# Kernel optimization log

Measured on AMD Instinct MI355X. Metric: run time of the kernel, lower is better.

Reference implementation:

```python
import jax, jax.numpy as jnp
import numpy as np

GRADIENT_SCALE = 1.0  # undefined global in the source; standard surrogate scale
ALPHA = 0.9
BETA = 0.8
THRESHOLD = 1.0
FEATURES = 512
UNITS = 1024
TIME = 256
BATCH = 128

@jax.custom_vjp
def heaviside(x):
    return jnp.where(x > 0, jnp.ones_like(x), jnp.zeros_like(x))

def _heaviside_fwd(x):
    return heaviside(x), x

def _heaviside_bwd(x, dy):
    # dy * GRADIENT_SCALE * (1/(|x|+1))^2  (surrogate gradient from tf.custom_gradient)
    return (dy * (GRADIENT_SCALE * jnp.square(1.0 / (jnp.abs(x) + 1.0))),)

heaviside.defvjp(_heaviside_fwd, _heaviside_bwd)


def setup_inputs() -> dict:
    key = jax.random.key(0)
    k1, k2 = jax.random.split(key)
    inputs = jax.random.normal(k1, (BATCH, FEATURES, TIME), dtype=jnp.float32)
    # keras add_weight default initializer ~ glorot_uniform; any float init is fine for a numerics baseline
    limit = np.sqrt(6.0 / (FEATURES + UNITS)).astype(np.float32)
    w = jax.random.uniform(k2, (FEATURES, UNITS), dtype=jnp.float32, minval=-limit, maxval=limit)
    return {"inputs": inputs, "w": w}


def reference(inputs, w):
    # In the original tf.while_loop body, membrane_potential, synapse and prev_s are
    # returned UNMODIFIED, so they remain zero for every timestep. The recurrence
    # therefore collapses exactly to, per step t:
    #   h_t = x[:, :, t] @ w
    #   i_t = alpha*0 + h_t = h_t
    #   v_t = (beta*0 + h_t) * (threshold - 0) = h_t * threshold
    #   s_t = heaviside(v_t - threshold)
    # which is timestep-independent and can be computed as one batched GEMM.
    h = jnp.einsum('bft,fu->btu', inputs, w)        # [B, T, U]
    v = (BETA * 0.0 + h) * (THRESHOLD - 0.0)        # state terms are identically zero
    s = heaviside(v - THRESHOLD)                    # [B, T, U]
    return jnp.transpose(s, (0, 2, 1))              # [B, U, T], matching tf transpose perm=[1,2,0]
```

## Files before the change

### kernel.cpp

```cpp
#include <hip/hip_runtime.h>


#define FF 512
#define TT 256
#define UU 1024
#define BK 8
#define MW 32

typedef float floatx16 __attribute__((ext_vector_type(16)));

__global__ __launch_bounds__(256, 6)
void snn_gemm_r5(const float* __restrict__ in, const float* __restrict__ w,
                 float* __restrict__ out) {
    const int b   = blockIdx.y;
    const int u0  = blockIdx.x * MW;
    const int tid = threadIdx.x;

    const float* __restrict__ inb = in + (size_t)b * FF * TT + tid;

    float acc[MW];
#pragma unroll
    for (int i = 0; i < MW; i++) acc[i] = 0.0f;

    float cur[BK], nxt[BK];
#pragma unroll
    for (int r = 0; r < BK; r++) cur[r] = inb[(size_t)r * TT];

    for (int f0 = 0; f0 < FF; f0 += BK) {
        if (f0 + BK < FF) {
#pragma unroll
            for (int r = 0; r < BK; r++)
                nxt[r] = inb[(size_t)(f0 + BK + r) * TT];
        }

#pragma unroll
        for (int k = 0; k < BK; k++) {
            const floatx16* __restrict__ pa =
                (const floatx16*)(w + (size_t)(f0 + k) * UU + u0);
            const floatx16 aL = pa[0];
            const floatx16 aH = pa[1];

            const float vb = cur[k];

#pragma unroll
            for (int i = 0; i < 16; i++)
                acc[i] = fmaf(aL[i], vb, acc[i]);
#pragma unroll
            for (int i = 0; i < 16; i++)
                acc[16 + i] = fmaf(aH[i], vb, acc[16 + i]);
        }

#pragma unroll
        for (int r = 0; r < BK; r++) cur[r] = nxt[r];
    }

    float* __restrict__ outb = out + ((size_t)b * UU + u0) * TT + tid;
#pragma unroll
    for (int i = 0; i < MW; i++)
        outb[(size_t)i * TT] = acc[i] > 1.0f ? 1.0f : 0.0f;
}

extern "C" void kernel_launch(void* const* d_in, const int* in_sizes, int n_in,
                              void* d_out, int out_size, void* d_ws, size_t ws_size,
                              hipStream_t stream) {
    const float* in = (const float*)d_in[0];
    const float* w  = (const float*)d_in[1];
    float* out      = (float*)d_out;

    dim3 grid(UU / MW, 128);
    snn_gemm_r5<<<grid, dim3(256), 0, stream>>>(in, w, out);
}
```

Baseline: 587.0 us.

## Restructure GEMM into LDS-tiled 128x64 blocks with async global-to-LDS double buffering

Replaces the per-thread column GEMM, where each thread kept 32 accumulators and streamed the weights through scalar or vector loads, with a 128(U) x 64(T) block tile. Each thread now computes a 16x8 register micro-tile from operands staged in shared memory, so each loaded value is reused across many FMAs. Tiles are loaded with global_load_lds into double-buffered LDS, and the output is written as float4 stores. The cost is higher register pressure (launch bounds drop to 2 blocks per CU) and a block-wide barrier every k-step, with no explicit wait on the async loads before the barrier.

```diff
diff --git a/kernel.cpp b/kernel.cpp
--- a/kernel.cpp
+++ b/kernel.cpp
@@ -5,59 +5,93 @@
 #define TT 256
 #define UU 1024
 #define BK 8
-#define MW 32
 
-typedef float floatx16 __attribute__((ext_vector_type(16)));
+__global__ __launch_bounds__(256, 2)
+void snn_gemm_r6(const float* __restrict__ in, const float* __restrict__ w,
+                 float* __restrict__ out) {
+    __shared__ float As[2][BK][128];
+    __shared__ float Bs[2][BK][64];
 
-__global__ __launch_bounds__(256, 6)
-void snn_gemm_r5(const float* __restrict__ in, const float* __restrict__ w,
-                 float* __restrict__ out) {
-    const int b   = blockIdx.y;
-    const int u0  = blockIdx.x * MW;
-    const int tid = threadIdx.x;
+    const int b    = blockIdx.z;
+    const int u0   = blockIdx.y * 128;
+    const int t0   = blockIdx.x * 64;
+    const int tid  = threadIdx.x;
+    const int wv   = tid >> 6;
+    const int lane = tid & 63;
+    const int g    = lane >> 3;
+    const int h    = lane & 7;
 
-    const float* __restrict__ inb = in + (size_t)b * FF * TT + tid;
+    const float* __restrict__ inb = in + (size_t)b * FF * TT;
 
-    float acc[MW];
+    float acc[16][8];
 #pragma unroll
-    for (int i = 0; i < MW; i++) acc[i] = 0.0f;
+    for (int i = 0; i < 16; i++)
+#pragma unroll
+        for (int j = 0; j < 8; j++) acc[i][j] = 0.0f;
 
-    float cur[BK], nxt[BK];
-#pragma unroll
-    for (int r = 0; r < BK; r++) cur[r] = inb[(size_t)r * TT];
+#define STAGE(fn, buf)                                                          \
+    do {                                                                        \
+        __builtin_amdgcn_global_load_lds(                                       \
+            (const __attribute__((address_space(1))) void*)                     \
+                (w + (size_t)((fn) + 2 * wv + (lane >> 5)) * UU + u0 +          \
+                 (lane & 31) * 4),                                              \
+            (__attribute__((address_space(3))) void*)&As[buf][2 * wv][0],       \
+            16, 0, 0);                                                          \
+        if (wv < 2) {                                                           \
+            __builtin_amdgcn_global_load_lds(                                   \
+                (const __attribute__((address_space(1))) void*)                 \
+                    (inb + (size_t)((fn) + 4 * wv + (lane >> 4)) * TT + t0 +    \
+                     (lane & 15) * 4),                                          \
+                (__attribute__((address_space(3))) void*)&Bs[buf][4 * wv][0],   \
+                16, 0, 0);                                                      \
+        }                                                                       \
+    } while (0)
+
+    STAGE(0, 0);
 
     for (int f0 = 0; f0 < FF; f0 += BK) {
-        if (f0 + BK < FF) {
-#pragma unroll
-            for (int r = 0; r < BK; r++)
-                nxt[r] = inb[(size_t)(f0 + BK + r) * TT];
-        }
+        const int buf = (f0 / BK) & 1;
+
+        __syncthreads();
+
+        if (f0 + BK < FF) STAGE(f0 + BK, buf ^ 1);
 
 #pragma unroll
         for (int k = 0; k < BK; k++) {
-            const floatx16* __restrict__ pa =
-                (const floatx16*)(w + (size_t)(f0 + k) * UU + u0);
-            const floatx16 aL = pa[0];
-            const floatx16 aH = pa[1];
+            const float4 a0 = *(const float4*)&As[buf][k][g * 8];
+            const float4 a1 = *(const float4*)&As[buf][k][g * 8 + 4];
+            const float4 a2 = *(const float4*)&As[buf][k][64 + g * 8];
+            const float4 a3 = *(const float4*)&As[buf][k][64 + g * 8 + 4];
+            const float4 b0 = *(const float4*)&Bs[buf][k][h * 4];
+            const float4 b1 = *(const float4*)&Bs[buf][k][32 + h * 4];
 
-            const float vb = cur[k];
+            const float am[16] = {a0.x, a0.y, a0.z, a0.w, a1.x, a1.y, a1.z, a1.w,
+                                  a2.x, a2.y, a2.z, a2.w, a3.x, a3.y, a3.z, a3.w};
+            const float bn[8]  = {b0.x, b0.y, b0.z, b0.w, b1.x, b1.y, b1.z, b1.w};
+#pragma unroll
+            for (int i = 0; i < 16; i++)
+#pragma unroll
+                for (int j = 0; j < 8; j++)
+                    acc[i][j] = fmaf(am[i], bn[j], acc[i][j]);
+        }
+    }
 
 #pragma unroll
-            for (int i = 0; i < 16; i++)
-                acc[i] = fmaf(aL[i], vb, acc[i]);
-#pragma unroll
-            for (int i = 0; i < 16; i++)
-                acc[16 + i] = fmaf(aH[i], vb, acc[16 + i]);
-        }
-
-#pragma unroll
-        for (int r = 0; r < BK; r++) cur[r] = nxt[r];
+    for (int i = 0; i < 16; i++) {
+        const int u = u0 + ((i < 8) ? (g * 8 + i) : (64 + g * 8 + i - 8));
+        float* __restrict__ orow = out + ((size_t)b * UU + u) * TT + t0;
+        float4 lo, hi;
+        lo.x = acc[i][0] > 1.0f ? 1.0f : 0.0f;
+        lo.y = acc[i][1] > 1.0f ? 1.0f : 0.0f;
+        lo.z = acc[i][2] > 1.0f ? 1.0f : 0.0f;
+        lo.w = acc[i][3] > 1.0f ? 1.0f : 0.0f;
+        hi.x = acc[i][4] > 1.0f ? 1.0f : 0.0f;
+        hi.y = acc[i][5] > 1.0f ? 1.0f : 0.0f;
+        hi.z = acc[i][6] > 1.0f ? 1.0f : 0.0f;
+        hi.w = acc[i][7] > 1.0f ? 1.0f : 0.0f;
+        *(float4*)&orow[h * 4]      = lo;
+        *(float4*)&orow[32 + h * 4] = hi;
     }
-
-    float* __restrict__ outb = out + ((size_t)b * UU + u0) * TT + tid;
-#pragma unroll
-    for (int i = 0; i < MW; i++)
-        outb[(size_t)i * TT] = acc[i] > 1.0f ? 1.0f : 0.0f;
 }
 
 extern "C" void kernel_launch(void* const* d_in, const int* in_sizes, int n_in,
@@ -67,6 +101,6 @@
     const float* w  = (const float*)d_in[1];
     float* out      = (float*)d_out;
 
-    dim3 grid(UU / MW, 128);
-    snn_gemm_r5<<<grid, dim3(256), 0, stream>>>(in, w, out);
+    dim3 grid(TT / 64, UU / 128, 128);
+    snn_gemm_r6<<<grid, dim3(256), 0, stream>>>(in, w, out);
 }
```

Measured after the change: 1.488 ms. 154% more time.
